# Kernel optimization log

Measured on AMD Instinct MI355X. Metric: run time of the kernel, lower is better.

Reference implementation:

```python
import jax, jax.numpy as jnp
import numpy as np

B, T, F, C, H = 256, 96, 256, 256, 512
NH, FFD = 8, 64  # transformer nhead=8, dim_feedforward=64 (PyPOTS defaults)


def make_pe(L, d):
    pos = np.arange(L)[:, None].astype(np.float32)
    div = np.exp(np.arange(0, d, 2).astype(np.float32) * (-np.log(10000.0) / d))
    pe = np.zeros((L, d), np.float32)
    pe[:, 0::2] = np.sin(pos * div)
    pe[:, 1::2] = np.cos(pos * div)
    return jnp.asarray(pe)


def setup_inputs() -> dict:
    key = jax.random.key(0)
    it = iter(jax.random.split(key, 64))

    def u(shape):
        s = 1.0 / np.sqrt(shape[-1])
        return jax.random.uniform(next(it), shape, jnp.float32, -s, s)

    return {
        "x": jax.random.normal(next(it), (B, T, F), jnp.float32),
        "mask": (jax.random.uniform(next(it), (B, T, F)) > 0.3).astype(jnp.float32),
        "deltas": jax.random.uniform(next(it), (B, T, F), jnp.float32) * 5.0,
        "last_obs": jax.random.normal(next(it), (B, T, F), jnp.float32),
        "intervals": jax.random.uniform(next(it), (F,), jnp.float32) * 2.0,
        "Wo": u((F, F)), "bo": jnp.zeros(F),            # Decay_obs linear
        "Wip": u((C, F)), "bip": jnp.zeros(C),          # input_projection (k=1 conv)
        "Wqkv": u((3 * C, C)), "bqkv": jnp.zeros(3 * C),
        "Wao": u((C, C)), "bao": jnp.zeros(C),
        "g1": jnp.ones(C), "be1": jnp.zeros(C),
        "W1": u((FFD, C)), "b1": jnp.zeros(FFD),
        "W2": u((C, FFD)), "b2": jnp.zeros(C),
        "g2": jnp.ones(C), "be2": jnp.zeros(C),
        "Wop1": u((H, C)), "bop1": jnp.zeros(H),        # output_projection1
        "wop2": u((2 * T,)), "bop2": jnp.zeros(1),      # output_projection2 (2T->1, k=1)
        "Wdh": u((H, F)), "bdh": jnp.zeros(H),          # temp_decay_h
        "wdx": u((F,)), "bdx": jnp.zeros(F),            # temp_decay_x (diag)
        "Wh": u((F, H)), "bh": jnp.zeros(F),            # hist
        "Wfr": u((F, F)), "bfr": jnp.zeros(F),          # feat_reg_v (off-diag mask)
        "Wwc": u((F, 2 * F)), "bwc": jnp.zeros(F),      # weight_combine
        "Wih": u((3 * H, 2 * F)), "bih": jnp.zeros(3 * H),
        "Whh": u((3 * H, H)), "bhh": jnp.zeros(3 * H),
    }


def layernorm(x, g, b):
    mu = jnp.mean(x, -1, keepdims=True)
    v = jnp.var(x, -1, keepdims=True)
    return (x - mu) * jax.lax.rsqrt(v + 1e-5) * g + b


def _forward(x, mask, deltas, last_obs, intervals, Wo, bo, Wip, bip, Wqkv, bqkv,
             Wao, bao, g1, be1, W1, b1, W2, b2, g2, be2, Wop1, bop1, wop2, bop2,
             Wdh, bdh, wdx, bdx, Wh, bh, Wfr, bfr, Wwc, bwc, Wih, bih, Whh, bhh):
    Bb, Tt, Ff = x.shape
    Cc = Wip.shape[0]
    DH = Cc // NH
    # --- Decay_obs: weight = 0.5 * (1 - tanh(sign(dd) * |W dd + b|)) ---
    dd = deltas - intervals[None, None, :]
    wd = dd @ Wo.T + bo
    decay_factor = 0.5 * (1.0 - jnp.tanh(jnp.sign(dd) * jnp.abs(wd)))
    # --- pre-encoder (h is None path) ---
    pe = make_pe(Tt, Cc)[None]                      # (1, T, C)
    d_lo = last_obs @ Wip.T + bip + pe
    d_df = decay_factor @ Wip.T + bip + pe
    data = jnp.concatenate([d_lo, d_df], axis=1)    # (B, 2T, C)
    # TransformerEncoderLayer(batch_first=False) on (B, 2T, C):
    # seq dim = axis 0 (batch), "batch" dim = axis 1 -- faithful to source quirk.
    qkv = data @ Wqkv.T + bqkv
    q, k, v = jnp.split(qkv, 3, axis=-1)
    q = q.reshape(Bb, 2 * Tt, NH, DH)
    k = k.reshape(Bb, 2 * Tt, NH, DH)
    v = v.reshape(Bb, 2 * Tt, NH, DH)
    scores = jnp.einsum('ilhd,jlhd->lhij', q, k) / float(np.sqrt(DH))
    attn = jax.nn.softmax(scores, axis=-1)
    ctx = jnp.einsum('lhij,jlhd->ilhd', attn, v).reshape(Bb, 2 * Tt, Cc)
    data = layernorm(data + ctx @ Wao.T + bao, g1, be1)
    ff = jax.nn.gelu(data @ W1.T + b1, approximate=False) @ W2.T + b2
    data = layernorm(data + ff, g2, be2)
    data = data @ Wop1.T + bop1                     # (B, 2T, H)
    h0 = jnp.einsum('blh,l->bh', data, wop2) + bop2 # output_projection2 -> (B, H)
    # --- sequential imputation loop ---
    Wfr_m = Wfr * (1.0 - jnp.eye(Ff, dtype=Wfr.dtype))
    def step(h, ts):
        x_t, d_t, m_t = ts
        gamma_h = jnp.exp(-jax.nn.relu(d_t @ Wdh.T + bdh))
        h = h * gamma_h
        x_h = h @ Wh.T + bh
        x_r = m_t * x_t + (1.0 - m_t) * x_h
        xu = x_r @ Wfr_m.T + bfr
        gamma_x = jnp.exp(-jax.nn.relu(d_t * wdx + bdx))
        beta = jnp.concatenate([gamma_x, m_t], axis=-1) @ Wwc.T + bwc
        x_comb = beta * xu + (1.0 - beta) * x_h
        loss = jnp.sum(jnp.abs(x_comb - x_t) * m_t) / (jnp.sum(m_t) + 1e-12)
        x_imp_t = m_t * x_t + (1.0 - m_t) * x_comb
        gi = jnp.concatenate([x_imp_t, m_t], axis=-1) @ Wih.T + bih
        gh = h @ Whh.T + bhh
        ir, iz, inn = jnp.split(gi, 3, axis=-1)
        hr, hz, hn = jnp.split(gh, 3, axis=-1)
        r = jax.nn.sigmoid(ir + hr)
        z = jax.nn.sigmoid(iz + hz)
        n = jnp.tanh(inn + r * hn)
        h_new = (1.0 - z) * n + z * h
        return h_new, (x_imp_t, x_comb, loss)

    xs = (jnp.swapaxes(x, 0, 1), jnp.swapaxes(deltas, 0, 1), jnp.swapaxes(mask, 0, 1))
    h_fin, (xi, rec, losses) = jax.lax.scan(step, h0, xs)
    x_imp = jnp.swapaxes(xi, 0, 1)
    reconstruction = jnp.swapaxes(rec, 0, 1)
    return x_imp, reconstruction, h_fin, jnp.sum(losses)


def reference(x, mask, deltas, last_obs, intervals, Wo, bo, Wip, bip, Wqkv, bqkv,
              Wao, bao, g1, be1, W1, b1, W2, b2, g2, be2, Wop1, bop1, wop2, bop2,
              Wdh, bdh, wdx, bdx, Wh, bh, Wfr, bfr, Wwc, bwc, Wih, bih, Whh, bhh):
    return _forward(x, mask, deltas, last_obs, intervals, Wo, bo, Wip, bip, Wqkv,
                    bqkv, Wao, bao, g1, be1, W1, b1, W2, b2, g2, be2, Wop1, bop1,
                    wop2, bop2, Wdh, bdh, wdx, bdx, Wh, bh, Wfr, bfr, Wwc, bwc,
                    Wih, bih, Whh, bhh)
```

## Files before the change

### kernel.cpp

```cpp
#include <hip/hip_runtime.h>
#include <cstdint>
#include <cstddef>

#define DEV __device__ __forceinline__

constexpr int Bb = 256, Tt = 96, Ff = 256, Cc = 256, Hh = 512;
constexpr int T2 = 192, FFDc = 64;

constexpr size_t SZ_DATA  = (size_t)Bb * T2 * Cc;
constexpr size_t SZ_QKV   = (size_t)Bb * T2 * 3 * Cc;
constexpr size_t OFF_DATA = 0;
constexpr size_t OFF_CTX  = OFF_DATA + SZ_DATA;
constexpr size_t OFF_QKV  = OFF_CTX + SZ_DATA;
constexpr size_t OFF_DF   = OFF_QKV;
constexpr size_t OFF_GAMH = OFF_QKV;
constexpr size_t OFF_BETA = OFF_QKV + (size_t)Bb * Tt * Hh;
constexpr size_t OFF_T1   = OFF_BETA + (size_t)Bb * Tt * Ff;
constexpr size_t OFF_S    = OFF_QKV + SZ_QKV;
constexpr size_t OFF_H    = OFF_S;
constexpr size_t OFF_DBAR = OFF_H    + (size_t)Bb * Hh;
constexpr size_t OFF_XHP  = OFF_DBAR + (size_t)Bb * Cc;
constexpr size_t OFF_GHP  = OFF_XHP  + 2 * (size_t)Bb * Ff;
constexpr size_t OFF_XUP  = OFF_GHP  + 2 * (size_t)Bb * 3 * Hh;
constexpr size_t OFF_XI   = OFF_XUP  + 4 * (size_t)Bb * Ff;
constexpr size_t OFF_GIP  = OFF_XI   + (size_t)Bb * Ff;
constexpr size_t OFF_LOSSP= OFF_GIP  + 2 * (size_t)Bb * 3 * Hh;
constexpr size_t OFF_DEN  = OFF_LOSSP + 256;
constexpr size_t OFF_SW   = OFF_DEN + 128;
constexpr size_t OFF_LOSS = OFF_SW + 4;
constexpr size_t WS_FLOATS = OFF_LOSS + 4;

template<int TN, class FA, class FB, class FE>
DEV void gemm_body(int kBegin, int kEnd, FA loadA, FB loadB, FE epi) {
  constexpr int BN = 16 * TN;
  __shared__ float As[16][68];
  __shared__ float Bs[16][BN + 4];
  const int tid = threadIdx.x;
  const int m0 = blockIdx.y * 64;
  const int n0 = blockIdx.x * BN;
  const int ty = tid >> 4, tx = tid & 15;
  float acc[4][TN];
#pragma unroll
  for (int i = 0; i < 4; i++)
#pragma unroll
    for (int j = 0; j < TN; j++) acc[i][j] = 0.f;

  for (int k0 = kBegin; k0 < kEnd; k0 += 16) {
    {
      const int lr = tid >> 2, lc = (tid & 3) * 4;
#pragma unroll
      for (int i = 0; i < 4; i++) As[lc + i][lr] = loadA(m0 + lr, k0 + lc + i);
    }
    if constexpr (TN == 4) {
      const int lr = tid >> 2, lc = (tid & 3) * 4;
#pragma unroll
      for (int i = 0; i < 4; i++) Bs[lc + i][lr] = loadB(n0 + lr, k0 + lc + i);
    } else {
      const int lr = tid >> 1, lc = (tid & 1) * 8;
#pragma unroll
      for (int i = 0; i < 8; i++) Bs[lc + i][lr] = loadB(n0 + lr, k0 + lc + i);
    }
    __syncthreads();
#pragma unroll
    for (int kk = 0; kk < 16; kk++) {
      float a[4], b[TN];
      float4 av = *(const float4*)&As[kk][ty * 4];
      a[0] = av.x; a[1] = av.y; a[2] = av.z; a[3] = av.w;
#pragma unroll
      for (int j = 0; j < TN; j += 4) {
        float4 bv = *(const float4*)&Bs[kk][tx * TN + j];
        b[j] = bv.x; b[j + 1] = bv.y; b[j + 2] = bv.z; b[j + 3] = bv.w;
      }
#pragma unroll
      for (int i = 0; i < 4; i++)
#pragma unroll
        for (int j = 0; j < TN; j++)
          acc[i][j] = fmaf(a[i], b[j], acc[i][j]);
    }
    __syncthreads();
  }
  epi(acc, m0 + ty * 4, n0 + tx * TN);
}

DEV float sigmoidf_(float v) { return 1.f / (1.f + __expf(-v)); }


__global__ __launch_bounds__(256) void k_decay(const float* __restrict__ deltas,
    const float* __restrict__ intervals, const float* __restrict__ Wo,
    const float* __restrict__ bo, float* __restrict__ df) {
  gemm_body<8>(0, 256,
    [&](int m, int k) { return deltas[(size_t)m * 256 + k] - intervals[k]; },
    [&](int n, int k) { return Wo[(size_t)n * 256 + k]; },
    [&](auto& acc, int mb, int nb) {
#pragma unroll
      for (int ii = 0; ii < 4; ii++)
#pragma unroll
        for (int jj = 0; jj < 8; jj++) {
          int m = mb + ii, n = nb + jj;
          float wd = acc[ii][jj] + bo[n];
          float dd = deltas[(size_t)m * 256 + n] - intervals[n];
          float sg = (dd > 0.f) ? 1.f : ((dd < 0.f) ? -1.f : 0.f);
          df[(size_t)m * 256 + n] = 0.5f * (1.f - tanhf(sg * fabsf(wd)));
        }
    });
}

__global__ __launch_bounds__(256) void k_proj(const float* __restrict__ A,
    const float* __restrict__ Wip, const float* __restrict__ bip,
    float* __restrict__ data, int hlf) {
  gemm_body<8>(0, 256,
    [&](int m, int k) { return A[(size_t)m * 256 + k]; },
    [&](int n, int k) { return Wip[(size_t)n * 256 + k]; },
    [&](auto& acc, int mb, int nb) {
#pragma unroll
      for (int ii = 0; ii < 4; ii++)
#pragma unroll
        for (int jj = 0; jj < 8; jj++) {
          int m = mb + ii, n = nb + jj;
          int b = m / 96, t = m % 96;
          float freq = __expf((float)(-(n & ~1)) * (9.210340371976184f / 256.f));
          float arg = (float)t * freq;
          float pe = (n & 1) ? cosf(arg) : sinf(arg);
          data[((size_t)b * 192 + hlf * 96 + t) * 256 + n] = acc[ii][jj] + bip[n] + pe;
        }
    });
}

__global__ __launch_bounds__(256) void k_qkv(const float* __restrict__ data,
    const float* __restrict__ Wqkv, const float* __restrict__ bqkv, float* __restrict__ qkv) {
  gemm_body<8>(0, 256,
    [&](int m, int k) { return data[(size_t)m * 256 + k]; },
    [&](int n, int k) { return Wqkv[(size_t)n * 256 + k]; },
    [&](auto& acc, int mb, int nb) {
#pragma unroll
      for (int ii = 0; ii < 4; ii++)
#pragma unroll
        for (int jj = 0; jj < 8; jj++) {
          int m = mb + ii, n = nb + jj;
          qkv[(size_t)m * 768 + n] = acc[ii][jj] + bqkv[n];
        }
    });
}

__global__ __launch_bounds__(256) void k_attn(const float* __restrict__ qkv, float* __restrict__ ctx) {
  const int bid = blockIdx.x;
  const int rb = bid & 3;
  const int h  = (bid >> 2) & 7;
  const int l  = bid >> 5;
  __shared__ float Qs[32][68];
  __shared__ float Ks[32][68];
  __shared__ float Vs[64][36];
  __shared__ float St[64][68];
  __shared__ float mrow[64], lrow[64], fscale[64], red[4][64];
  const int tid = threadIdx.x;
  {
    int i = tid & 63, dg = tid >> 6;
    const float* src = qkv + ((size_t)(rb * 64 + i) * 192 + l) * 768 + h * 32 + dg * 8;
    float4 v0 = *(const float4*)src;
    float4 v1 = *(const float4*)(src + 4);
    int d0 = dg * 8;
    Qs[d0 + 0][i] = v0.x; Qs[d0 + 1][i] = v0.y; Qs[d0 + 2][i] = v0.z; Qs[d0 + 3][i] = v0.w;
    Qs[d0 + 4][i] = v1.x; Qs[d0 + 5][i] = v1.y; Qs[d0 + 6][i] = v1.z; Qs[d0 + 7][i] = v1.w;
  }
  if (tid < 64) { mrow[tid] = -1e30f; lrow[tid] = 0.f; }
  float accO[4][4] = {{0.f}};
  const int sm_i = tid & 63, sm_jq = tid >> 6;
  const int pv_i0 = (tid & 15) * 4, pv_d0 = ((tid >> 4) & 7) * 4;
  const bool pv_on = tid < 128;

  for (int jb = 0; jb < 4; jb++) {
    {
      int j = tid & 63, dg = tid >> 6;
      const float* srcK = qkv + ((size_t)(jb * 64 + j) * 192 + l) * 768 + 256 + h * 32 + dg * 8;
      float4 v0 = *(const float4*)srcK;
      float4 v1 = *(const float4*)(srcK + 4);
      int d0 = dg * 8;
      Ks[d0 + 0][j] = v0.x; Ks[d0 + 1][j] = v0.y; Ks[d0 + 2][j] = v0.z; Ks[d0 + 3][j] = v0.w;
      Ks[d0 + 4][j] = v1.x; Ks[d0 + 5][j] = v1.y; Ks[d0 + 6][j] = v1.z; Ks[d0 + 7][j] = v1.w;
      const float* srcV = srcK + 256;
      float4 w0 = *(const float4*)srcV;
      float4 w1 = *(const float4*)(srcV + 4);
      *(float4*)&Vs[j][d0] = w0;
      *(float4*)&Vs[j][d0 + 4] = w1;
    }
    __syncthreads();
    {
      const int j0 = (tid >> 4) * 4, i0 = (tid & 15) * 4;
      float sacc[4][4] = {{0.f}};
#pragma unroll
      for (int k = 0; k < 32; k++) {
        float4 a = *(const float4*)&Ks[k][j0];
        float4 b = *(const float4*)&Qs[k][i0];
        float aa[4] = {a.x, a.y, a.z, a.w}, bb[4] = {b.x, b.y, b.z, b.w};
// ... 14 lines not shown
#pragma unroll
    for (int jj = 0; jj < 16; jj++) pm = fmaxf(pm, St[sm_jq * 16 + jj][sm_i]);
    red[sm_jq][sm_i] = pm;
    __syncthreads();
    float m_new = fmaxf(mrow[sm_i], fmaxf(fmaxf(red[0][sm_i], red[1][sm_i]), fmaxf(red[2][sm_i], red[3][sm_i])));
    __syncthreads();
    float psum = 0.f;
#pragma unroll
    for (int jj = 0; jj < 16; jj++) {
      float e = __expf(St[sm_jq * 16 + jj][sm_i] - m_new);
      St[sm_jq * 16 + jj][sm_i] = e;
      psum += e;
    }
    red[sm_jq][sm_i] = psum;
    if (sm_jq == 0) fscale[sm_i] = __expf(mrow[sm_i] - m_new);
    __syncthreads();
    if (sm_jq == 0) {
      lrow[sm_i] = lrow[sm_i] * fscale[sm_i] + red[0][sm_i] + red[1][sm_i] + red[2][sm_i] + red[3][sm_i];
      mrow[sm_i] = m_new;
    }
    if (pv_on) {
#pragma unroll
      for (int ii = 0; ii < 4; ii++) {
        float f = fscale[pv_i0 + ii];
#pragma unroll
        for (int dd = 0; dd < 4; dd++) accO[ii][dd] *= f;
      }
      for (int j = 0; j < 64; j++) {
        float4 a = *(const float4*)&St[j][pv_i0];
        float4 b = *(const float4*)&Vs[j][pv_d0];
        float aa[4] = {a.x, a.y, a.z, a.w}, bb[4] = {b.x, b.y, b.z, b.w};
#pragma unroll
        for (int ii = 0; ii < 4; ii++)
#pragma unroll
          for (int dd = 0; dd < 4; dd++)
            accO[ii][dd] = fmaf(aa[ii], bb[dd], accO[ii][dd]);
      }
    }
    __syncthreads();
  }
  if (pv_on) {
#pragma unroll
    for (int ii = 0; ii < 4; ii++) {
      float inv = 1.f / lrow[pv_i0 + ii];
#pragma unroll
      for (int dd = 0; dd < 4; dd++)
        ctx[((size_t)(rb * 64 + pv_i0 + ii) * 192 + l) * 256 + h * 32 + pv_d0 + dd] = accO[ii][dd] * inv;
    }
  }
}

__global__ __launch_bounds__(256) void k_attnout(const float* __restrict__ ctx,
    const float* __restrict__ Wao, const float* __restrict__ bao, float* __restrict__ data) {
  gemm_body<8>(0, 256,
    [&](int m, int k) { return ctx[(size_t)m * 256 + k]; },
    [&](int n, int k) { return Wao[(size_t)n * 256 + k]; },
    [&](auto& acc, int mb, int nb) {
#pragma unroll
      for (int ii = 0; ii < 4; ii++)
#pragma unroll
        for (int jj = 0; jj < 8; jj++) {
          int m = mb + ii, n = nb + jj;
          data[(size_t)m * 256 + n] += acc[ii][jj] + bao[n];
        }
    });
}

__global__ __launch_bounds__(256) void k_ln(float* __restrict__ data,
    const float* __restrict__ g, const float* __restrict__ b) {
  int row = blockIdx.x * 4 + (threadIdx.x >> 6);
  int lane = threadIdx.x & 63;
  float* p = data + (size_t)row * 256;
  float4 v = *(float4*)&p[lane * 4];
  float s = v.x + v.y + v.z + v.w;
  float q = v.x * v.x + v.y * v.y + v.z * v.z + v.w * v.w;
  for (int o = 32; o >= 1; o >>= 1) { s += __shfl_xor(s, o); q += __shfl_xor(q, o); }
  float mu = s * (1.f / 256.f);
  float var = q * (1.f / 256.f) - mu * mu;
  float inv = rsqrtf(var + 1e-5f);
  int c = lane * 4;
  v.x = (v.x - mu) * inv * g[c + 0] + b[c + 0];
  v.y = (v.y - mu) * inv * g[c + 1] + b[c + 1];
  v.z = (v.z - mu) * inv * g[c + 2] + b[c + 2];
  v.w = (v.w - mu) * inv * g[c + 3] + b[c + 3];
  *(float4*)&p[lane * 4] = v;
}

__global__ __launch_bounds__(256) void k_ff1(const float* __restrict__ data,
    const float* __restrict__ W1, const float* __restrict__ b1, float* __restrict__ t1) {
  gemm_body<4>(0, 256,
    [&](int m, int k) { return data[(size_t)m * 256 + k]; },
    [&](int n, int k) { return W1[(size_t)n * 256 + k]; },
    [&](auto& acc, int mb, int nb) {
#pragma unroll
      for (int ii = 0; ii < 4; ii++)
#pragma unroll
        for (int jj = 0; jj < 4; jj++) {
          int m = mb + ii, n = nb + jj;
          float v = acc[ii][jj] + b1[n];
          v = 0.5f * v * (1.f + erff(v * 0.7071067811865476f));
          t1[(size_t)m * 64 + n] = v;
        }
    });
}

__global__ __launch_bounds__(256) void k_ff2(const float* __restrict__ t1,
    const float* __restrict__ W2, const float* __restrict__ b2, float* __restrict__ data) {
  gemm_body<8>(0, 64,
    [&](int m, int k) { return t1[(size_t)m * 64 + k]; },
    [&](int n, int k) { return W2[(size_t)n * 64 + k]; },
    [&](auto& acc, int mb, int nb) {
#pragma unroll
      for (int ii = 0; ii < 4; ii++)
#pragma unroll
        for (int jj = 0; jj < 8; jj++) {
          int m = mb + ii, n = nb + jj;
          data[(size_t)m * 256 + n] += acc[ii][jj] + b2[n];
        }
    });
}

__global__ __launch_bounds__(256) void k_dbar(const float* __restrict__ data,
    const float* __restrict__ wop2, float* __restrict__ dbar, float* __restrict__ sw) {
  int b = blockIdx.x, c = threadIdx.x;
  float acc = 0.f;
  for (int lq = 0; lq < 192; lq++) acc += wop2[lq] * data[((size_t)b * 192 + lq) * 256 + c];
  dbar[(size_t)b * 256 + c] = acc;
  if (b == 0 && c == 0) {
    float s = 0.f;
    for (int lq = 0; lq < 192; lq++) s += wop2[lq];
    sw[0] = s;
  }
}

__global__ __launch_bounds__(256) void k_h0(const float* __restrict__ dbar,
    const float* __restrict__ Wop1, const float* __restrict__ bop1,
    const float* __restrict__ bop2, const float* __restrict__ sw, float* __restrict__ h) {
  gemm_body<4>(0, 256,
    [&](int m, int k) { return dbar[(size_t)m * 256 + k]; },
    [&](int n, int k) { return Wop1[(size_t)n * 256 + k]; },
    [&](auto& acc, int mb, int nb) {
#pragma unroll
      for (int ii = 0; ii < 4; ii++)
#pragma unroll
        for (int jj = 0; jj < 4; jj++) {
          int m = mb + ii, n = nb + jj;
          h[(size_t)m * 512 + n] = acc[ii][jj] + sw[0] * bop1[n] + bop2[0];
        }
    });
}

__global__ __launch_bounds__(256) void k_gamh(const float* __restrict__ deltas,
    const float* __restrict__ Wdh, const float* __restrict__ bdh, float* __restrict__ gamH) {
  gemm_body<8>(0, 256,
    [&](int m, int k) { return deltas[(size_t)m * 256 + k]; },
    [&](int n, int k) { return Wdh[(size_t)n * 256 + k]; },
    [&](auto& acc, int mb, int nb) {
#pragma unroll
      for (int ii = 0; ii < 4; ii++)
#pragma unroll
        for (int jj = 0; jj < 8; jj++) {
          int m = mb + ii, n = nb + jj;
          gamH[(size_t)m * 512 + n] = __expf(-fmaxf(acc[ii][jj] + bdh[n], 0.f));
        }
    });
}

__global__ __launch_bounds__(256) void k_beta(const float* __restrict__ deltas,
    const float* __restrict__ mask, const float* __restrict__ wdx, const float* __restrict__ bdx,
    const float* __restrict__ Wwc, const float* __restrict__ bwc, float* __restrict__ beta) {
  gemm_body<8>(0, 512,
    [&](int m, int k) {
      if (k < 256) {
        float d = deltas[(size_t)m * 256 + k];
        return __expf(-fmaxf(fmaf(d, wdx[k], bdx[k]), 0.f));
      }
      return mask[(size_t)m * 256 + (k - 256)];
    },
    [&](int n, int k) { return Wwc[(size_t)n * 512 + k]; },
    [&](auto& acc, int mb, int nb) {
#pragma unroll
      for (int ii = 0; ii < 4; ii++)
#pragma unroll
        for (int jj = 0; jj < 8; jj++) {
          int m = mb + ii, n = nb + jj;
          beta[(size_t)m * 256 + n] = acc[ii][jj] + bwc[n];
        }
    });
}

__global__ __launch_bounds__(256) void k_den(const float* __restrict__ mask, float* __restrict__ den) {
  int t = blockIdx.x, tid = threadIdx.x;
  float s = 0.f;
  for (int idx = tid; idx < 256 * 256; idx += 256) {
    int b = idx >> 8, f = idx & 255;
    s += mask[((size_t)b * 96 + t) * 256 + f];
  }
  for (int o = 32; o >= 1; o >>= 1) s += __shfl_xor(s, o);
  __shared__ float rs[4];
  if ((tid & 63) == 0) rs[tid >> 6] = s;
  __syncthreads();
  if (tid == 0) den[t] = rs[0] + rs[1] + rs[2] + rs[3] + 1e-12f;
}


__global__ __launch_bounds__(256) void k_p1(const float* __restrict__ h,
    const float* __restrict__ gamH, const float* __restrict__ Wh, const float* __restrict__ Whh,
    float* __restrict__ xh_p, float* __restrict__ gh_p, int t) {
  const int z = blockIdx.z;
  gemm_body<4>(z * 256, z * 256 + 256,
    [&](int m, int k) { return h[(size_t)m * 512 + k] * gamH[((size_t)m * 96 + t) * 512 + k]; },
    [&](int n, int k) { return (n < 256) ? Wh[(size_t)n * 512 + k] : Whh[(size_t)(n - 256) * 512 + k]; },
    [&](auto& acc, int mb, int nb) {
#pragma unroll
      for (int ii = 0; ii < 4; ii++)
#pragma unroll
        for (int jj = 0; jj < 4; jj++) {
          int m = mb + ii, n = nb + jj;
          if (n < 256) xh_p[(size_t)z * 65536 + (size_t)m * 256 + n] = acc[ii][jj];
          else gh_p[(size_t)z * 393216 + (size_t)m * 1536 + (n - 256)] = acc[ii][jj];
        }
    });
}

__global__ __launch_bounds__(256) void k_p2(const float* __restrict__ mask,
    const float* __restrict__ x, const float* __restrict__ xh_p, const float* __restrict__ bh,
    const float* __restrict__ Wfr, float* __restrict__ xu_p, int t) {
  const int z = blockIdx.z;
  gemm_body<4>(z * 64, z * 64 + 64,
    [&](int m, int k) {
      size_t i3 = ((size_t)m * 96 + t) * 256 + k;
      float mk = mask[i3];
      float xh = xh_p[(size_t)m * 256 + k] + xh_p[65536 + (size_t)m * 256 + k] + bh[k];
      return mk * x[i3] + (1.f - mk) * xh;
    },
    [&](int n, int k) { float w = Wfr[(size_t)n * 256 + k]; return (n == k) ? 0.f : w; },
    [&](auto& acc, int mb, int nb) {
#pragma unroll
      for (int ii = 0; ii < 4; ii++)
#pragma unroll
        for (int jj = 0; jj < 4; jj++) {
          int m = mb + ii, n = nb + jj;
          xu_p[(size_t)z * 65536 + (size_t)m * 256 + n] = acc[ii][jj];
        }
    });
}

__global__ __launch_bounds__(256) void k_p2b(const float* __restrict__ xu_p,
    const float* __restrict__ xh_p, const float* __restrict__ bh, const float* __restrict__ bfr,
    const float* __restrict__ beta, const float* __restrict__ mask, const float* __restrict__ x,
    float* __restrict__ out_ximp, float* __restrict__ out_rec, float* __restrict__ xi,
    float* __restrict__ lossp, int t) {
  int e = blockIdx.x * 256 + threadIdx.x;
  int m = e >> 8, f = e & 255;
  size_t i3 = ((size_t)m * 96 + t) * 256 + f;
  float xu = xu_p[e] + xu_p[65536 + e] + xu_p[131072 + e] + xu_p[196608 + e] + bfr[f];
  float xh = xh_p[e] + xh_p[65536 + e] + bh[f];
  float bt = beta[i3];
  float xc = bt * xu + (1.f - bt) * xh;
  float mk = mask[i3], xv = x[i3];
  float xim = mk * xv + (1.f - mk) * xc;
  out_ximp[i3] = xim;
  out_rec[i3] = xc;
  xi[e] = xim;
  float pl = fabsf(xc - xv) * mk;
  for (int o = 32; o >= 1; o >>= 1) pl += __shfl_xor(pl, o);
  __shared__ float rs[4];
  if ((threadIdx.x & 63) == 0) rs[threadIdx.x >> 6] = pl;
  __syncthreads();
  if (threadIdx.x == 0) lossp[blockIdx.x] = rs[0] + rs[1] + rs[2] + rs[3];
}

__global__ __launch_bounds__(256) void k_p3(const float* __restrict__ xi,
    const float* __restrict__ mask, const float* __restrict__ Wih,
    float* __restrict__ gi_p, int t) {
  const int z = blockIdx.z;
  gemm_body<4>(z * 256, z * 256 + 256,
    [&](int m, int k) {
      if (k < 256) return xi[(size_t)m * 256 + k];
      return mask[((size_t)m * 96 + t) * 256 + (k - 256)];
    },
    [&](int n, int k) { return Wih[(size_t)n * 512 + k]; },
    [&](auto& acc, int mb, int nb) {
#pragma unroll
      for (int ii = 0; ii < 4; ii++)
#pragma unroll
        for (int jj = 0; jj < 4; jj++) {
          int m = mb + ii, n = nb + jj;
          gi_p[(size_t)z * 393216 + (size_t)m * 1536 + n] = acc[ii][jj];
        }
    });
}

__global__ __launch_bounds__(256) void k_pd(float* __restrict__ h,
    const float* __restrict__ gamH, const float* __restrict__ gi_p, const float* __restrict__ gh_p,
    const float* __restrict__ bih, const float* __restrict__ bhh,
    const float* __restrict__ lossp, float* __restrict__ lossacc,
    const float* __restrict__ den, int t) {
  if (blockIdx.x == 512) {
    float s = lossp[threadIdx.x];
    for (int o = 32; o >= 1; o >>= 1) s += __shfl_xor(s, o);
    __shared__ float rs[4];
    if ((threadIdx.x & 63) == 0) rs[threadIdx.x >> 6] = s;
    __syncthreads();
    if (threadIdx.x == 0) lossacc[0] += (rs[0] + rs[1] + rs[2] + rs[3]) / den[t];
    return;
  }
  int e = blockIdx.x * 256 + threadIdx.x;
  int m = e >> 9, j = e & 511;
  float gam = gamH[((size_t)m * 96 + t) * 512 + j];
  float hd = h[e] * gam;
  size_t b0 = (size_t)m * 1536 + j;
  float ir  = gi_p[b0]        + gi_p[393216 + b0]        + bih[j];
  float iz  = gi_p[b0 + 512]  + gi_p[393216 + b0 + 512]  + bih[j + 512];
  float in_ = gi_p[b0 + 1024] + gi_p[393216 + b0 + 1024] + bih[j + 1024];
  float hr  = gh_p[b0]        + gh_p[393216 + b0]        + bhh[j];
  float hz  = gh_p[b0 + 512]  + gh_p[393216 + b0 + 512]  + bhh[j + 512];
  float hn  = gh_p[b0 + 1024] + gh_p[393216 + b0 + 1024] + bhh[j + 1024];
  float r = sigmoidf_(ir + hr);
  float z = sigmoidf_(iz + hz);
  float nn = tanhf(in_ + r * hn);
  h[e] = (1.f - z) * nn + z * hd;
}

extern "C" void kernel_launch(void* const* d_in, const int* in_sizes, int n_in,
                              void* d_out, int out_size, void* d_ws, size_t ws_size,
                              hipStream_t stream) {
  if (ws_size < WS_FLOATS * sizeof(float)) return;

  const float* x        = (const float*)d_in[0];
  const float* mask     = (const float*)d_in[1];
  const float* deltas   = (const float*)d_in[2];
  const float* last_obs = (const float*)d_in[3];
  const float* intervals= (const float*)d_in[4];
  const float* Wo  = (const float*)d_in[5];
  const float* bo  = (const float*)d_in[6];
  const float* Wip = (const float*)d_in[7];
  const float* bip = (const float*)d_in[8];
  const float* Wqkv= (const float*)d_in[9];
  const float* bqkv= (const float*)d_in[10];
  const float* Wao = (const float*)d_in[11];
  const float* bao = (const float*)d_in[12];
  const float* g1  = (const float*)d_in[13];
  const float* be1 = (const float*)d_in[14];
  const float* W1  = (const float*)d_in[15];
  const float* b1  = (const float*)d_in[16];
  const float* W2  = (const float*)d_in[17];
  const float* b2  = (const float*)d_in[18];
  const float* g2  = (const float*)d_in[19];
  const float* be2 = (const float*)d_in[20];
  const float* Wop1= (const float*)d_in[21];
  const float* bop1= (const float*)d_in[22];
  const float* wop2= (const float*)d_in[23];
  const float* bop2= (const float*)d_in[24];
  const float* Wdh = (const float*)d_in[25];
  const float* bdh = (const float*)d_in[26];
  const float* wdx = (const float*)d_in[27];
  const float* bdx = (const float*)d_in[28];
  const float* Wh  = (const float*)d_in[29];
  const float* bh  = (const float*)d_in[30];
  const float* Wfr = (const float*)d_in[31];
  const float* bfr = (const float*)d_in[32];
  const float* Wwc = (const float*)d_in[33];
  const float* bwc = (const float*)d_in[34];
  const float* Wih = (const float*)d_in[35];
  const float* bih = (const float*)d_in[36];
  const float* Whh = (const float*)d_in[37];
  const float* bhh = (const float*)d_in[38];

  float* out = (float*)d_out;
  float* ws  = (float*)d_ws;
  float* data  = ws + OFF_DATA;
  float* ctx   = ws + OFF_CTX;
  float* qkv   = ws + OFF_QKV;
  float* df    = ws + OFF_DF;
  float* gamH  = ws + OFF_GAMH;
  float* beta  = ws + OFF_BETA;
  float* t1    = ws + OFF_T1;
  float* h     = ws + OFF_H;
  float* dbar  = ws + OFF_DBAR;
  float* xh_p  = ws + OFF_XHP;
  float* gh_p  = ws + OFF_GHP;
  float* xu_p  = ws + OFF_XUP;
  float* xi    = ws + OFF_XI;
  float* gi_p  = ws + OFF_GIP;
  float* lossp = ws + OFF_LOSSP;
  float* den   = ws + OFF_DEN;
  float* sw    = ws + OFF_SW;
  float* lossacc = ws + OFF_LOSS;

  float* out_ximp = out;
  float* out_rec  = out + (size_t)Bb * Tt * Ff;
  float* out_h    = out + 2 * (size_t)Bb * Tt * Ff;
  float* out_loss = out_h + (size_t)Bb * Hh;

  const dim3 blk(256);

  k_decay<<<dim3(2, 384), blk, 0, stream>>>(deltas, intervals, Wo, bo, df);
  k_proj<<<dim3(2, 384), blk, 0, stream>>>(last_obs, Wip, bip, data, 0);
  k_proj<<<dim3(2, 384), blk, 0, stream>>>(df, Wip, bip, data, 1);
  k_qkv<<<dim3(6, 768), blk, 0, stream>>>(data, Wqkv, bqkv, qkv);
  k_attn<<<dim3(6144), blk, 0, stream>>>(qkv, ctx);
  k_attnout<<<dim3(2, 768), blk, 0, stream>>>(ctx, Wao, bao, data);
  k_ln<<<dim3(12288), blk, 0, stream>>>(data, g1, be1);
  k_ff1<<<dim3(1, 768), blk, 0, stream>>>(data, W1, b1, t1);
  k_ff2<<<dim3(2, 768), blk, 0, stream>>>(t1, W2, b2, data);
  k_ln<<<dim3(12288), blk, 0, stream>>>(data, g2, be2);
  k_dbar<<<dim3(256), blk, 0, stream>>>(data, wop2, dbar, sw);
  k_h0<<<dim3(8, 4), blk, 0, stream>>>(dbar, Wop1, bop1, bop2, sw, h);

  k_gamh<<<dim3(4, 384), blk, 0, stream>>>(deltas, Wdh, bdh, gamH);
  k_beta<<<dim3(2, 384), blk, 0, stream>>>(deltas, mask, wdx, bdx, Wwc, bwc, beta);
  k_den<<<dim3(96), blk, 0, stream>>>(mask, den);
  hipMemsetAsync(lossacc, 0, sizeof(float), stream);

  for (int t = 0; t < 96; t++) {
    k_p1<<<dim3(32, 4, 2), blk, 0, stream>>>(h, gamH, Wh, Whh, xh_p, gh_p, t);
    k_p2<<<dim3(4, 4, 4), blk, 0, stream>>>(mask, x, xh_p, bh, Wfr, xu_p, t);
    k_p2b<<<dim3(256), blk, 0, stream>>>(xu_p, xh_p, bh, bfr, beta, mask, x,
                                         out_ximp, out_rec, xi, lossp, t);
    k_p3<<<dim3(24, 4, 2), blk, 0, stream>>>(xi, mask, Wih, gi_p, t);
    k_pd<<<dim3(513), blk, 0, stream>>>(h, gamH, gi_p, gh_p, bih, bhh, lossp, lossacc, den, t);
  }

  hipMemcpyAsync(out_h, h, (size_t)Bb * Hh * sizeof(float), hipMemcpyDeviceToDevice, stream);
  hipMemcpyAsync(out_loss, lossacc, sizeof(float), hipMemcpyDeviceToDevice, stream);
}
```

Measured before the change: 6.381 ms.

## Use split-bf16 MFMA GEMMs and fuse recurrent-step kernels without split-K

```diff
diff --git a/kernel.cpp b/kernel.cpp
--- a/kernel.cpp
+++ b/kernel.cpp
@@ -4,8 +4,13 @@
 
 #define DEV __device__ __forceinline__
 
+typedef __attribute__((ext_vector_type(8))) short short8;
+typedef __attribute__((ext_vector_type(4))) float f32x4;
+typedef unsigned int uint;
+typedef unsigned short ushort;
+
 constexpr int Bb = 256, Tt = 96, Ff = 256, Cc = 256, Hh = 512;
-constexpr int T2 = 192, FFDc = 64;
+constexpr int T2 = 192;
 
 constexpr size_t SZ_DATA  = (size_t)Bb * T2 * Cc;
 constexpr size_t SZ_QKV   = (size_t)Bb * T2 * 3 * Cc;
@@ -19,126 +24,155 @@
 constexpr size_t OFF_S    = OFF_QKV + SZ_QKV;
 constexpr size_t OFF_H    = OFF_S;
 constexpr size_t OFF_DBAR = OFF_H    + (size_t)Bb * Hh;
-constexpr size_t OFF_XHP  = OFF_DBAR + (size_t)Bb * Cc;
-constexpr size_t OFF_GHP  = OFF_XHP  + 2 * (size_t)Bb * Ff;
-constexpr size_t OFF_XUP  = OFF_GHP  + 2 * (size_t)Bb * 3 * Hh;
-constexpr size_t OFF_XI   = OFF_XUP  + 4 * (size_t)Bb * Ff;
-constexpr size_t OFF_GIP  = OFF_XI   + (size_t)Bb * Ff;
-constexpr size_t OFF_LOSSP= OFF_GIP  + 2 * (size_t)Bb * 3 * Hh;
+constexpr size_t OFF_XH   = OFF_DBAR + (size_t)Bb * Cc;
+constexpr size_t OFF_GH   = OFF_XH   + (size_t)Bb * Ff;
+constexpr size_t OFF_XI   = OFF_GH   + (size_t)Bb * 3 * Hh;
+constexpr size_t OFF_LOSSP= OFF_XI   + (size_t)Bb * Ff;
 constexpr size_t OFF_DEN  = OFF_LOSSP + 256;
 constexpr size_t OFF_SW   = OFF_DEN + 128;
 constexpr size_t OFF_LOSS = OFF_SW + 4;
 constexpr size_t WS_FLOATS = OFF_LOSS + 4;
 
-template<int TN, class FA, class FB, class FE>
-DEV void gemm_body(int kBegin, int kEnd, FA loadA, FB loadB, FE epi) {
-  constexpr int BN = 16 * TN;
-  __shared__ float As[16][68];
-  __shared__ float Bs[16][BN + 4];
+DEV ushort f2bf(float f) {
+  uint u = __float_as_uint(f);
+  u += 0x7fffu + ((u >> 16) & 1u);
+  return (ushort)(u >> 16);
+}
+DEV float bf2f(ushort b) { return __uint_as_float(((uint)b) << 16); }
+DEV float sigmoidf_(float v) { return 1.f / (1.f + __expf(-v)); }
+
+template<int GN, class FA, class FB, class FE>
+DEV void mgemm(int K, FA loadA, FB loadB, FE epi) {
+  __shared__ __align__(16) ushort As[128][64];
+  __shared__ __align__(16) ushort Bs[GN][64][64];
   const int tid = threadIdx.x;
-  const int m0 = blockIdx.y * 64;
-  const int n0 = blockIdx.x * BN;
-  const int ty = tid >> 4, tx = tid & 15;
-  float acc[4][TN];
-#pragma unroll
-  for (int i = 0; i < 4; i++)
-#pragma unroll
-    for (int j = 0; j < TN; j++) acc[i][j] = 0.f;
-
-  for (int k0 = kBegin; k0 < kEnd; k0 += 16) {
-    {
-      const int lr = tid >> 2, lc = (tid & 3) * 4;
-#pragma unroll
-      for (int i = 0; i < 4; i++) As[lc + i][lr] = loadA(m0 + lr, k0 + lc + i);
-    }
-    if constexpr (TN == 4) {
-      const int lr = tid >> 2, lc = (tid & 3) * 4;
-#pragma unroll
-      for (int i = 0; i < 4; i++) Bs[lc + i][lr] = loadB(n0 + lr, k0 + lc + i);
-    } else {
-      const int lr = tid >> 1, lc = (tid & 1) * 8;
-#pragma unroll
-      for (int i = 0; i < 8; i++) Bs[lc + i][lr] = loadB(n0 + lr, k0 + lc + i);
-    }
-    __syncthreads();
-#pragma unroll
-    for (int kk = 0; kk < 16; kk++) {
-      float a[4], b[TN];
-      float4 av = *(const float4*)&As[kk][ty * 4];
-      a[0] = av.x; a[1] = av.y; a[2] = av.z; a[3] = av.w;
-#pragma unroll
-      for (int j = 0; j < TN; j += 4) {
-        float4 bv = *(const float4*)&Bs[kk][tx * TN + j];
-        b[j] = bv.x; b[j + 1] = bv.y; b[j + 2] = bv.z; b[j + 3] = bv.w;
-      }
-#pragma unroll
-      for (int i = 0; i < 4; i++)
-#pragma unroll
-        for (int j = 0; j < TN; j++)
-          acc[i][j] = fmaf(a[i], b[j], acc[i][j]);
-    }
-    __syncthreads();
-  }
-  epi(acc, m0 + ty * 4, n0 + tx * TN);
-}
-
-DEV float sigmoidf_(float v) { return 1.f / (1.f + __expf(-v)); }
+  const int m0 = blockIdx.y * 128, n0 = blockIdx.x * 64;
+  const int w = tid >> 6, l = tid & 63;
+  f32x4 acc[GN][2][4];
+#pragma unroll
+  for (int g = 0; g < GN; g++)
+#pragma unroll
+    for (int rb = 0; rb < 2; rb++)
+#pragma unroll
+      for (int nb = 0; nb < 4; nb++)
+        acc[g][rb][nb] = (f32x4){0.f, 0.f, 0.f, 0.f};
+
+  for (int k0 = 0; k0 < K; k0 += 32) {
+#pragma unroll
+    for (int i = 0; i < 2; i++) {
+      int ch = tid * 2 + i;
+      int row = ch >> 2, c = ch & 3;
+      short8 hv, lv;
+#pragma unroll
+      for (int j = 0; j < 8; j++) {
+        float v = loadA(m0 + row, k0 + c * 8 + j);
+        ushort hb = f2bf(v);
+        ushort lb = f2bf(v - bf2f(hb));
+        hv[j] = (short)hb; lv[j] = (short)lb;
+      }
+      int hs = c ^ (row & 7);
+      *(short8*)&As[row][hs * 8] = hv;
+      *(short8*)&As[row][(hs ^ 4) * 8] = lv;
+    }
+#pragma unroll
+    for (int g = 0; g < GN; g++) {
+      int row = tid >> 2, c = tid & 3;
+      short8 hv, lv;
+#pragma unroll
+      for (int j = 0; j < 8; j++) {
+        float v = loadB(g, n0 + row, k0 + c * 8 + j);
+        ushort hb = f2bf(v);
+        ushort lb = f2bf(v - bf2f(hb));
+        hv[j] = (short)hb; lv[j] = (short)lb;
+      }
+      int hs = c ^ (row & 7);
+      *(short8*)&Bs[g][row][hs * 8] = hv;
+      *(short8*)&Bs[g][row][(hs ^ 4) * 8] = lv;
+    }
+    __syncthreads();
+    const int c = l >> 4;
+    short8 ah[2], al[2];
+#pragma unroll
+    for (int rb = 0; rb < 2; rb++) {
+      int r = w * 32 + rb * 16 + (l & 15);
+      int hs = c ^ (r & 7);
+      ah[rb] = *(const short8*)&As[r][hs * 8];
+      al[rb] = *(const short8*)&As[r][(hs ^ 4) * 8];
+    }
+#pragma unroll
+    for (int g = 0; g < GN; g++) {
+      short8 bh[4], bl[4];
+#pragma unroll
+      for (int nb = 0; nb < 4; nb++) {
+        int r = nb * 16 + (l & 15);
+        int hs = c ^ (r & 7);
+        bh[nb] = *(const short8*)&Bs[g][r][hs * 8];
+        bl[nb] = *(const short8*)&Bs[g][r][(hs ^ 4) * 8];
+      }
+#pragma unroll
+      for (int rb = 0; rb < 2; rb++)
+#pragma unroll
+        for (int nb = 0; nb < 4; nb++) {
+          f32x4 a = acc[g][rb][nb];
+          a = __builtin_amdgcn_mfma_f32_16x16x32_bf16(ah[rb], bh[nb], a, 0, 0, 0);
+          a = __builtin_amdgcn_mfma_f32_16x16x32_bf16(ah[rb], bl[nb], a, 0, 0, 0);
+          a = __builtin_amdgcn_mfma_f32_16x16x32_bf16(al[rb], bh[nb], a, 0, 0, 0);
+          acc[g][rb][nb] = a;
+        }
+    }
+    __syncthreads();
+  }
+#pragma unroll
+  for (int rb = 0; rb < 2; rb++)
+#pragma unroll
+    for (int nb = 0; nb < 4; nb++)
+#pragma unroll
+      for (int reg = 0; reg < 4; reg++) {
+        float vals[GN];
+#pragma unroll
+        for (int g = 0; g < GN; g++) vals[g] = acc[g][rb][nb][reg];
+        epi(vals, m0 + w * 32 + rb * 16 + ((l >> 4) << 2) + reg,
+            n0 + nb * 16 + (l & 15));
+      }
+}
 
 
 __global__ __launch_bounds__(256) void k_decay(const float* __restrict__ deltas,
     const float* __restrict__ intervals, const float* __restrict__ Wo,
     const float* __restrict__ bo, float* __restrict__ df) {
-  gemm_body<8>(0, 256,
+  mgemm<1>(256,
     [&](int m, int k) { return deltas[(size_t)m * 256 + k] - intervals[k]; },
-    [&](int n, int k) { return Wo[(size_t)n * 256 + k]; },
-    [&](auto& acc, int mb, int nb) {
-#pragma unroll
-      for (int ii = 0; ii < 4; ii++)
-#pragma unroll
-        for (int jj = 0; jj < 8; jj++) {
-          int m = mb + ii, n = nb + jj;
-          float wd = acc[ii][jj] + bo[n];
-          float dd = deltas[(size_t)m * 256 + n] - intervals[n];
-          float sg = (dd > 0.f) ? 1.f : ((dd < 0.f) ? -1.f : 0.f);
-          df[(size_t)m * 256 + n] = 0.5f * (1.f - tanhf(sg * fabsf(wd)));
-        }
+    [&](int g, int n, int k) { return Wo[(size_t)n * 256 + k]; },
+    [&](float (&v)[1], int m, int n) {
+      float wd = v[0] + bo[n];
+      float dd = deltas[(size_t)m * 256 + n] - intervals[n];
+      float sg = (dd > 0.f) ? 1.f : ((dd < 0.f) ? -1.f : 0.f);
+      df[(size_t)m * 256 + n] = 0.5f * (1.f - tanhf(sg * fabsf(wd)));
     });
 }
 
 __global__ __launch_bounds__(256) void k_proj(const float* __restrict__ A,
     const float* __restrict__ Wip, const float* __restrict__ bip,
     float* __restrict__ data, int hlf) {
-  gemm_body<8>(0, 256,
+  mgemm<1>(256,
     [&](int m, int k) { return A[(size_t)m * 256 + k]; },
-    [&](int n, int k) { return Wip[(size_t)n * 256 + k]; },
-    [&](auto& acc, int mb, int nb) {
-#pragma unroll
-      for (int ii = 0; ii < 4; ii++)
-#pragma unroll
-        for (int jj = 0; jj < 8; jj++) {
-          int m = mb + ii, n = nb + jj;
-          int b = m / 96, t = m % 96;
-          float freq = __expf((float)(-(n & ~1)) * (9.210340371976184f / 256.f));
-          float arg = (float)t * freq;
-          float pe = (n & 1) ? cosf(arg) : sinf(arg);
-          data[((size_t)b * 192 + hlf * 96 + t) * 256 + n] = acc[ii][jj] + bip[n] + pe;
-        }
+    [&](int g, int n, int k) { return Wip[(size_t)n * 256 + k]; },
+    [&](float (&v)[1], int m, int n) {
+      int b = m / 96, t = m % 96;
+      float freq = __expf((float)(-(n & ~1)) * (9.210340371976184f / 256.f));
+      float arg = (float)t * freq;
+      float pe = (n & 1) ? cosf(arg) : sinf(arg);
+      data[((size_t)b * 192 + hlf * 96 + t) * 256 + n] = v[0] + bip[n] + pe;
     });
 }
 
 __global__ __launch_bounds__(256) void k_qkv(const float* __restrict__ data,
     const float* __restrict__ Wqkv, const float* __restrict__ bqkv, float* __restrict__ qkv) {
-  gemm_body<8>(0, 256,
+  mgemm<1>(256,
     [&](int m, int k) { return data[(size_t)m * 256 + k]; },
-    [&](int n, int k) { return Wqkv[(size_t)n * 256 + k]; },
-    [&](auto& acc, int mb, int nb) {
-#pragma unroll
-      for (int ii = 0; ii < 4; ii++)
-#pragma unroll
-        for (int jj = 0; jj < 8; jj++) {
-          int m = mb + ii, n = nb + jj;
-          qkv[(size_t)m * 768 + n] = acc[ii][jj] + bqkv[n];
-        }
+    [&](int g, int n, int k) { return Wqkv[(size_t)n * 256 + k]; },
+    [&](float (&v)[1], int m, int n) {
+      qkv[(size_t)m * 768 + n] = v[0] + bqkv[n];
     });
 }
 
@@ -259,17 +293,11 @@
 
 __global__ __launch_bounds__(256) void k_attnout(const float* __restrict__ ctx,
     const float* __restrict__ Wao, const float* __restrict__ bao, float* __restrict__ data) {
-  gemm_body<8>(0, 256,
+  mgemm<1>(256,
     [&](int m, int k) { return ctx[(size_t)m * 256 + k]; },
-    [&](int n, int k) { return Wao[(size_t)n * 256 + k]; },
-    [&](auto& acc, int mb, int nb) {
-#pragma unroll
-      for (int ii = 0; ii < 4; ii++)
-#pragma unroll
-        for (int jj = 0; jj < 8; jj++) {
-          int m = mb + ii, n = nb + jj;
-          data[(size_t)m * 256 + n] += acc[ii][jj] + bao[n];
-        }
+    [&](int g, int n, int k) { return Wao[(size_t)n * 256 + k]; },
+    [&](float (&v)[1], int m, int n) {
+      data[(size_t)m * 256 + n] += v[0] + bao[n];
     });
 }
 
@@ -295,35 +323,23 @@
 
 __global__ __launch_bounds__(256) void k_ff1(const float* __restrict__ data,
     const float* __restrict__ W1, const float* __restrict__ b1, float* __restrict__ t1) {
-  gemm_body<4>(0, 256,
+  mgemm<1>(256,
     [&](int m, int k) { return data[(size_t)m * 256 + k]; },
-    [&](int n, int k) { return W1[(size_t)n * 256 + k]; },
-    [&](auto& acc, int mb, int nb) {
-#pragma unroll
-      for (int ii = 0; ii < 4; ii++)
-#pragma unroll
-        for (int jj = 0; jj < 4; jj++) {
-          int m = mb + ii, n = nb + jj;
-          float v = acc[ii][jj] + b1[n];
-          v = 0.5f * v * (1.f + erff(v * 0.7071067811865476f));
-          t1[(size_t)m * 64 + n] = v;
-        }
+    [&](int g, int n, int k) { return W1[(size_t)n * 256 + k]; },
+    [&](float (&v)[1], int m, int n) {
+      float u = v[0] + b1[n];
+      u = 0.5f * u * (1.f + erff(u * 0.7071067811865476f));
+      t1[(size_t)m * 64 + n] = u;
     });
 }
 
 __global__ __launch_bounds__(256) void k_ff2(const float* __restrict__ t1,
     const float* __restrict__ W2, const float* __restrict__ b2, float* __restrict__ data) {
-  gemm_body<8>(0, 64,
+  mgemm<1>(64,
     [&](int m, int k) { return t1[(size_t)m * 64 + k]; },
-    [&](int n, int k) { return W2[(size_t)n * 64 + k]; },
-    [&](auto& acc, int mb, int nb) {
-#pragma unroll
-      for (int ii = 0; ii < 4; ii++)
-#pragma unroll
-        for (int jj = 0; jj < 8; jj++) {
-          int m = mb + ii, n = nb + jj;
-          data[(size_t)m * 256 + n] += acc[ii][jj] + b2[n];
-        }
+    [&](int g, int n, int k) { return W2[(size_t)n * 64 + k]; },
+    [&](float (&v)[1], int m, int n) {
+      data[(size_t)m * 256 + n] += v[0] + b2[n];
     });
 }
 
@@ -343,40 +359,28 @@
 __global__ __launch_bounds__(256) void k_h0(const float* __restrict__ dbar,
     const float* __restrict__ Wop1, const float* __restrict__ bop1,
     const float* __restrict__ bop2, const float* __restrict__ sw, float* __restrict__ h) {
-  gemm_body<4>(0, 256,
+  mgemm<1>(256,
     [&](int m, int k) { return dbar[(size_t)m * 256 + k]; },
-    [&](int n, int k) { return Wop1[(size_t)n * 256 + k]; },
-    [&](auto& acc, int mb, int nb) {
-#pragma unroll
-      for (int ii = 0; ii < 4; ii++)
-#pragma unroll
-        for (int jj = 0; jj < 4; jj++) {
-          int m = mb + ii, n = nb + jj;
-          h[(size_t)m * 512 + n] = acc[ii][jj] + sw[0] * bop1[n] + bop2[0];
-        }
+    [&](int g, int n, int k) { return Wop1[(size_t)n * 256 + k]; },
+    [&](float (&v)[1], int m, int n) {
+      h[(size_t)m * 512 + n] = v[0] + sw[0] * bop1[n] + bop2[0];
     });
 }
 
 __global__ __launch_bounds__(256) void k_gamh(const float* __restrict__ deltas,
     const float* __restrict__ Wdh, const float* __restrict__ bdh, float* __restrict__ gamH) {
-  gemm_body<8>(0, 256,
+  mgemm<1>(256,
     [&](int m, int k) { return deltas[(size_t)m * 256 + k]; },
-    [&](int n, int k) { return Wdh[(size_t)n * 256 + k]; },
-    [&](auto& acc, int mb, int nb) {
-#pragma unroll
-      for (int ii = 0; ii < 4; ii++)
-#pragma unroll
-        for (int jj = 0; jj < 8; jj++) {
-          int m = mb + ii, n = nb + jj;
-          gamH[(size_t)m * 512 + n] = __expf(-fmaxf(acc[ii][jj] + bdh[n], 0.f));
-        }
+    [&](int g, int n, int k) { return Wdh[(size_t)n * 256 + k]; },
+    [&](float (&v)[1], int m, int n) {
+      gamH[(size_t)m * 512 + n] = __expf(-fmaxf(v[0] + bdh[n], 0.f));
     });
 }
 
 __global__ __launch_bounds__(256) void k_beta(const float* __restrict__ deltas,
     const float* __restrict__ mask, const float* __restrict__ wdx, const float* __restrict__ bdx,
     const float* __restrict__ Wwc, const float* __restrict__ bwc, float* __restrict__ beta) {
-  gemm_body<8>(0, 512,
+  mgemm<1>(512,
     [&](int m, int k) {
       if (k < 256) {
         float d = deltas[(size_t)m * 256 + k];
@@ -384,15 +388,9 @@
       }
       return mask[(size_t)m * 256 + (k - 256)];
     },
-    [&](int n, int k) { return Wwc[(size_t)n * 512 + k]; },
-    [&](auto& acc, int mb, int nb) {
-#pragma unroll
-      for (int ii = 0; ii < 4; ii++)
-#pragma unroll
-        for (int jj = 0; jj < 8; jj++) {
-          int m = mb + ii, n = nb + jj;
-          beta[(size_t)m * 256 + n] = acc[ii][jj] + bwc[n];
-        }
+    [&](int g, int n, int k) { return Wwc[(size_t)n * 512 + k]; },
+    [&](float (&v)[1], int m, int n) {
+      beta[(size_t)m * 256 + n] = v[0] + bwc[n];
     });
 }
 
@@ -413,121 +411,78 @@
 
 __global__ __launch_bounds__(256) void k_p1(const float* __restrict__ h,
     const float* __restrict__ gamH, const float* __restrict__ Wh, const float* __restrict__ Whh,
-    float* __restrict__ xh_p, float* __restrict__ gh_p, int t) {
-  const int z = blockIdx.z;
-  gemm_body<4>(z * 256, z * 256 + 256,
+    float* __restrict__ xh, float* __restrict__ gh, int t) {
+  mgemm<1>(512,
     [&](int m, int k) { return h[(size_t)m * 512 + k] * gamH[((size_t)m * 96 + t) * 512 + k]; },
-    [&](int n, int k) { return (n < 256) ? Wh[(size_t)n * 512 + k] : Whh[(size_t)(n - 256) * 512 + k]; },
-    [&](auto& acc, int mb, int nb) {
-#pragma unroll
-      for (int ii = 0; ii < 4; ii++)
-#pragma unroll
-        for (int jj = 0; jj < 4; jj++) {
-          int m = mb + ii, n = nb + jj;
-          if (n < 256) xh_p[(size_t)z * 65536 + (size_t)m * 256 + n] = acc[ii][jj];
-          else gh_p[(size_t)z * 393216 + (size_t)m * 1536 + (n - 256)] = acc[ii][jj];
-        }
+    [&](int g, int n, int k) {
+      return (n < 256) ? Wh[(size_t)n * 512 + k] : Whh[(size_t)(n - 256) * 512 + k];
+    },
+    [&](float (&v)[1], int m, int n) {
+      if (n < 256) xh[(size_t)m * 256 + n] = v[0];
+      else gh[(size_t)m * 1536 + (n - 256)] = v[0];
     });
 }
 
 __global__ __launch_bounds__(256) void k_p2(const float* __restrict__ mask,
-    const float* __restrict__ x, const float* __restrict__ xh_p, const float* __restrict__ bh,
-    const float* __restrict__ Wfr, float* __restrict__ xu_p, int t) {
-  const int z = blockIdx.z;
-  gemm_body<4>(z * 64, z * 64 + 64,
+    const float* __restrict__ x, const float* __restrict__ xh, const float* __restrict__ bh,
+    const float* __restrict__ Wfr, const float* __restrict__ bfr,
+    const float* __restrict__ beta, float* __restrict__ out_ximp, float* __restrict__ out_rec,
+    float* __restrict__ xi, float* __restrict__ lossp, int t) {
+  float lsum = 0.f;
+  mgemm<1>(256,
     [&](int m, int k) {
       size_t i3 = ((size_t)m * 96 + t) * 256 + k;
       float mk = mask[i3];
-      float xh = xh_p[(size_t)m * 256 + k] + xh_p[65536 + (size_t)m * 256 + k] + bh[k];
-      return mk * x[i3] + (1.f - mk) * xh;
+      float xhv = xh[(size_t)m * 256 + k] + bh[k];
+      return mk * x[i3] + (1.f - mk) * xhv;
     },
-    [&](int n, int k) { float w = Wfr[(size_t)n * 256 + k]; return (n == k) ? 0.f : w; },
-    [&](auto& acc, int mb, int nb) {
-#pragma unroll
-      for (int ii = 0; ii < 4; ii++)
-#pragma unroll
-        for (int jj = 0; jj < 4; jj++) {
-          int m = mb + ii, n = nb + jj;
-          xu_p[(size_t)z * 65536 + (size_t)m * 256 + n] = acc[ii][jj];
-        }
-    });
-}
-
-__global__ __launch_bounds__(256) void k_p2b(const float* __restrict__ xu_p,
-    const float* __restrict__ xh_p, const float* __restrict__ bh, const float* __restrict__ bfr,
-    const float* __restrict__ beta, const float* __restrict__ mask, const float* __restrict__ x,
-    float* __restrict__ out_ximp, float* __restrict__ out_rec, float* __restrict__ xi,
-    float* __restrict__ lossp, int t) {
-  int e = blockIdx.x * 256 + threadIdx.x;
-  int m = e >> 8, f = e & 255;
-  size_t i3 = ((size_t)m * 96 + t) * 256 + f;
-  float xu = xu_p[e] + xu_p[65536 + e] + xu_p[131072 + e] + xu_p[196608 + e] + bfr[f];
-  float xh = xh_p[e] + xh_p[65536 + e] + bh[f];
-  float bt = beta[i3];
-  float xc = bt * xu + (1.f - bt) * xh;
-  float mk = mask[i3], xv = x[i3];
-  float xim = mk * xv + (1.f - mk) * xc;
-  out_ximp[i3] = xim;
-  out_rec[i3] = xc;
-  xi[e] = xim;
-  float pl = fabsf(xc - xv) * mk;
-  for (int o = 32; o >= 1; o >>= 1) pl += __shfl_xor(pl, o);
+    [&](int g, int n, int k) { float w = Wfr[(size_t)n * 256 + k]; return (n == k) ? 0.f : w; },
+    [&](float (&v)[1], int m, int n) {
+      size_t i3 = ((size_t)m * 96 + t) * 256 + n;
+      float xu = v[0] + bfr[n];
+      float xhv = xh[(size_t)m * 256 + n] + bh[n];
+      float bt = beta[i3];
+      float xc = bt * xu + (1.f - bt) * xhv;
+      float mk = mask[i3], xv = x[i3];
+      float xim = mk * xv + (1.f - mk) * xc;
+      out_ximp[i3] = xim;
+      out_rec[i3] = xc;
+      xi[(size_t)m * 256 + n] = xim;
+      lsum += fabsf(xc - xv) * mk;
+    });
+  for (int o = 32; o >= 1; o >>= 1) lsum += __shfl_xor(lsum, o);
   __shared__ float rs[4];
-  if ((threadIdx.x & 63) == 0) rs[threadIdx.x >> 6] = pl;
+  if ((threadIdx.x & 63) == 0) rs[threadIdx.x >> 6] = lsum;
   __syncthreads();
-  if (threadIdx.x == 0) lossp[blockIdx.x] = rs[0] + rs[1] + rs[2] + rs[3];
+  if (threadIdx.x == 0) lossp[blockIdx.y * 4 + blockIdx.x] = rs[0] + rs[1] + rs[2] + rs[3];
 }
 
 __global__ __launch_bounds__(256) void k_p3(const float* __restrict__ xi,
     const float* __restrict__ mask, const float* __restrict__ Wih,
-    float* __restrict__ gi_p, int t) {
-  const int z = blockIdx.z;
-  gemm_body<4>(z * 256, z * 256 + 256,
+    const float* __restrict__ bih, const float* __restrict__ bhh,
+    const float* __restrict__ gh, const float* __restrict__ gamH,
+    float* __restrict__ h, const float* __restrict__ lossp, float* __restrict__ lossacc,
+    const float* __restrict__ den, int t) {
+  if (blockIdx.x == 0 && blockIdx.y == 0 && threadIdx.x == 0) {
+    float s = 0.f;
+    for (int i = 0; i < 8; i++) s += lossp[i];
+    lossacc[0] += s / den[t];
+  }
+  mgemm<3>(512,
     [&](int m, int k) {
-      if (k < 256) return xi[(size_t)m * 256 + k];
-      return mask[((size_t)m * 96 + t) * 256 + (k - 256)];
+      return (k < 256) ? xi[(size_t)m * 256 + k]
+                       : mask[((size_t)m * 96 + t) * 256 + (k - 256)];
     },
-    [&](int n, int k) { return Wih[(size_t)n * 512 + k]; },
-    [&](auto& acc, int mb, int nb) {
-#pragma unroll
-      for (int ii = 0; ii < 4; ii++)
-#pragma unroll
-        for (int jj = 0; jj < 4; jj++) {
-          int m = mb + ii, n = nb + jj;
-          gi_p[(size_t)z * 393216 + (size_t)m * 1536 + n] = acc[ii][jj];
-        }
-    });
-}
-
-__global__ __launch_bounds__(256) void k_pd(float* __restrict__ h,
-    const float* __restrict__ gamH, const float* __restrict__ gi_p, const float* __restrict__ gh_p,
-    const float* __restrict__ bih, const float* __restrict__ bhh,
-    const float* __restrict__ lossp, float* __restrict__ lossacc,
-    const float* __restrict__ den, int t) {
-  if (blockIdx.x == 512) {
-    float s = lossp[threadIdx.x];
-    for (int o = 32; o >= 1; o >>= 1) s += __shfl_xor(s, o);
-    __shared__ float rs[4];
-    if ((threadIdx.x & 63) == 0) rs[threadIdx.x >> 6] = s;
-    __syncthreads();
-    if (threadIdx.x == 0) lossacc[0] += (rs[0] + rs[1] + rs[2] + rs[3]) / den[t];
-    return;
-  }
-  int e = blockIdx.x * 256 + threadIdx.x;
-  int m = e >> 9, j = e & 511;
-  float gam = gamH[((size_t)m * 96 + t) * 512 + j];
-  float hd = h[e] * gam;
-  size_t b0 = (size_t)m * 1536 + j;
-  float ir  = gi_p[b0]        + gi_p[393216 + b0]        + bih[j];
-  float iz  = gi_p[b0 + 512]  + gi_p[393216 + b0 + 512]  + bih[j + 512];
-  float in_ = gi_p[b0 + 1024] + gi_p[393216 + b0 + 1024] + bih[j + 1024];
-  float hr  = gh_p[b0]        + gh_p[393216 + b0]        + bhh[j];
-  float hz  = gh_p[b0 + 512]  + gh_p[393216 + b0 + 512]  + bhh[j + 512];
-  float hn  = gh_p[b0 + 1024] + gh_p[393216 + b0 + 1024] + bhh[j + 1024];
-  float r = sigmoidf_(ir + hr);
-  float z = sigmoidf_(iz + hz);
-  float nn = tanhf(in_ + r * hn);
-  h[e] = (1.f - z) * nn + z * hd;
+    [&](int g, int n, int k) { return Wih[((size_t)n + (size_t)g * 512) * 512 + k]; },
+    [&](float (&v)[3], int m, int j) {
+      size_t gb = (size_t)m * 1536 + j;
+      float gam = gamH[((size_t)m * 96 + t) * 512 + j];
+      float hd = h[(size_t)m * 512 + j] * gam;
+      float r = sigmoidf_(v[0] + bih[j] + gh[gb] + bhh[j]);
+      float z = sigmoidf_(v[1] + bih[j + 512] + gh[gb + 512] + bhh[j + 512]);
+      float nn = tanhf(v[2] + bih[j + 1024] + r * (gh[gb + 1024] + bhh[j + 1024]));
+      h[(size_t)m * 512 + j] = (1.f - z) * nn + z * hd;
+    });
 }
 
 extern "C" void kernel_launch(void* const* d_in, const int* in_sizes, int n_in,
@@ -586,11 +541,9 @@
   float* t1    = ws + OFF_T1;
   float* h     = ws + OFF_H;
   float* dbar  = ws + OFF_DBAR;
-  float* xh_p  = ws + OFF_XHP;
-  float* gh_p  = ws + OFF_GHP;
-  float* xu_p  = ws + OFF_XUP;
+  float* xh    = ws + OFF_XH;
+  float* gh    = ws + OFF_GH;
   float* xi    = ws + OFF_XI;
-  float* gi_p  = ws + OFF_GIP;
   float* lossp = ws + OFF_LOSSP;
   float* den   = ws + OFF_DEN;
   float* sw    = ws + OFF_SW;
@@ -603,31 +556,30 @@
 
   const dim3 blk(256);
 
-  k_decay<<<dim3(2, 384), blk, 0, stream>>>(deltas, intervals, Wo, bo, df);
-  k_proj<<<dim3(2, 384), blk, 0, stream>>>(last_obs, Wip, bip, data, 0);
-  k_proj<<<dim3(2, 384), blk, 0, stream>>>(df, Wip, bip, data, 1);
-  k_qkv<<<dim3(6, 768), blk, 0, stream>>>(data, Wqkv, bqkv, qkv);
+  k_decay<<<dim3(4, 192), blk, 0, stream>>>(deltas, intervals, Wo, bo, df);
+  k_proj<<<dim3(4, 192), blk, 0, stream>>>(last_obs, Wip, bip, data, 0);
+  k_proj<<<dim3(4, 192), blk, 0, stream>>>(df, Wip, bip, data, 1);
+  k_qkv<<<dim3(12, 384), blk, 0, stream>>>(data, Wqkv, bqkv, qkv);
   k_attn<<<dim3(6144), blk, 0, stream>>>(qkv, ctx);
-  k_attnout<<<dim3(2, 768), blk, 0, stream>>>(ctx, Wao, bao, data);
+  k_attnout<<<dim3(4, 768), blk, 0, stream>>>(ctx, Wao, bao, data);
   k_ln<<<dim3(12288), blk, 0, stream>>>(data, g1, be1);
-  k_ff1<<<dim3(1, 768), blk, 0, stream>>>(data, W1, b1, t1);
-  k_ff2<<<dim3(2, 768), blk, 0, stream>>>(t1, W2, b2, data);
+  k_ff1<<<dim3(1, 384), blk, 0, stream>>>(data, W1, b1, t1);
+  k_ff2<<<dim3(4, 384), blk, 0, stream>>>(t1, W2, b2, data);
   k_ln<<<dim3(12288), blk, 0, stream>>>(data, g2, be2);
   k_dbar<<<dim3(256), blk, 0, stream>>>(data, wop2, dbar, sw);
-  k_h0<<<dim3(8, 4), blk, 0, stream>>>(dbar, Wop1, bop1, bop2, sw, h);
-
-  k_gamh<<<dim3(4, 384), blk, 0, stream>>>(deltas, Wdh, bdh, gamH);
-  k_beta<<<dim3(2, 384), blk, 0, stream>>>(deltas, mask, wdx, bdx, Wwc, bwc, beta);
+  k_h0<<<dim3(8, 2), blk, 0, stream>>>(dbar, Wop1, bop1, bop2, sw, h);
+
+  k_gamh<<<dim3(8, 192), blk, 0, stream>>>(deltas, Wdh, bdh, gamH);
+  k_beta<<<dim3(4, 192), blk, 0, stream>>>(deltas, mask, wdx, bdx, Wwc, bwc, beta);
   k_den<<<dim3(96), blk, 0, stream>>>(mask, den);
   hipMemsetAsync(lossacc, 0, sizeof(float), stream);
 
   for (int t = 0; t < 96; t++) {
-    k_p1<<<dim3(32, 4, 2), blk, 0, stream>>>(h, gamH, Wh, Whh, xh_p, gh_p, t);
-    k_p2<<<dim3(4, 4, 4), blk, 0, stream>>>(mask, x, xh_p, bh, Wfr, xu_p, t);
-    k_p2b<<<dim3(256), blk, 0, stream>>>(xu_p, xh_p, bh, bfr, beta, mask, x,
+    k_p1<<<dim3(28, 2), blk, 0, stream>>>(h, gamH, Wh, Whh, xh, gh, t);
+    k_p2<<<dim3(4, 2), blk, 0, stream>>>(mask, x, xh, bh, Wfr, bfr, beta,
                                          out_ximp, out_rec, xi, lossp, t);
-    k_p3<<<dim3(24, 4, 2), blk, 0, stream>>>(xi, mask, Wih, gi_p, t);
-    k_pd<<<dim3(513), blk, 0, stream>>>(h, gamH, gi_p, gh_p, bih, bhh, lossp, lossacc, den, t);
+    k_p3<<<dim3(8, 2), blk, 0, stream>>>(xi, mask, Wih, bih, bhh, gh, gamH,
+                                         h, lossp, lossacc, den, t);
   }
 
   hipMemcpyAsync(out_h, h, (size_t)Bb * Hh * sizeof(float), hipMemcpyDeviceToDevice, stream);
```

New measurement: 10.80 ms. +69.2%, slower.
